# Performance work log

Hardware: AMD Instinct MI355X
Metric: run time of the kernel (lower is better)

## Reference

```python
import jax, jax.numpy as jnp
import numpy as np

B = 1024          # number of graphs
N = 64            # atoms per graph
NUM_NODES = B * N
HID = 256         # hidden_channels
H1 = HID // 2
E = 2_097_152     # edges (avg degree 32)


def _xavier(k, fan_in, fan_out):
    lim = np.sqrt(6.0 / (fan_in + fan_out)).astype(np.float32)
    return jax.random.uniform(k, (fan_in, fan_out), jnp.float32, -lim, lim)


def setup_inputs() -> dict:
    key = jax.random.key(0)
    ks = jax.random.split(key, 6)
    node_features = jax.random.normal(ks[0], (NUM_NODES, HID), jnp.float32)
    edge_index = jax.random.randint(ks[1], (2, E), 0, NUM_NODES)
    batch = jnp.repeat(jnp.arange(B), N)  # sorted graph ids, equal-size graphs
    W1 = _xavier(ks[2], HID + 1, H1); b1 = jnp.zeros((H1,), jnp.float32)
    W2 = _xavier(ks[3], H1, H1);      b2 = jnp.zeros((H1,), jnp.float32)
    W3 = _xavier(ks[4], H1, 1);       b3 = jnp.zeros((1,), jnp.float32)
    kT = jnp.ones((1,), jnp.float32)
    return {"node_features": node_features, "W1": W1, "b1": b1, "W2": W2,
            "b2": b2, "W3": W3, "b3": b3, "kT": kT,
            "edge_index": edge_index, "batch": batch}


def reference(node_features, W1, b1, W2, b2, W3, b3, kT, edge_index, batch):
    num_nodes = node_features.shape[0]
    # node degree: count of occurrences as source node
    deg = jnp.zeros((num_nodes,), jnp.float32).at[edge_index[0]].add(1.0)
    # per-graph atom counts and segment start offsets (n_atoms_i)
    counts = jax.ops.segment_sum(jnp.ones((num_nodes,), jnp.float32), batch,
                                 num_segments=B)
    start = jnp.cumsum(counts) - counts  # exclusive cumsum
    # stable per-graph sort of degrees in one shot: lexsort keys, primary=batch
    order = jnp.lexsort((deg, batch))  # global original indices, sorted by (batch, deg)
    # connectivity feature: local original index of the k-th smallest-degree
    # node in its graph, normalized by graph size (matches sorted_index / n_atoms_i)
    conn = (order.astype(jnp.float32) - start[batch]) / counts[batch]
    # MLP(hidden+1 -> hid/2 -> hid/2 -> 1) with silu
    x = jnp.concatenate([conn[:, None], node_features], axis=-1)  # [nodes, HID+1]
    h = jax.nn.silu(x @ W1 + b1)
    h = jax.nn.silu(h @ W2 + b2)
    logits = (h @ W3 + b3)[:, 0] / kT[0]
    # per-graph (segment) softmax
    m = jax.ops.segment_max(logits, batch, num_segments=B)
    e = jnp.exp(logits - m[batch])
    s = jax.ops.segment_sum(e, batch, num_segments=B)
    return e / s[batch]  # concat of per-graph softmaxed probabilities
```

## Files before the change

### kernel.cpp

```cpp
#include <hip/hip_runtime.h>

#define NB 1024
#define NPG 64
#define NUM_NODES 65536
#define HID 256
#define H1DIM 128
#define NE 2097152

typedef __attribute__((ext_vector_type(8))) _Float16 f16x8;
typedef __attribute__((ext_vector_type(4))) float f32x4;

#define W2F_HALF 32768
#define DEGF_OFF (96*1024)
#define PART_OFF (352*1024)

__global__ void wprep_kernel(const float* __restrict__ W1,
                             const float* __restrict__ W2,
                             _Float16* __restrict__ wf) {
    const int b = blockIdx.x;
    const int t = threadIdx.x;
    const int L = t & 63;
    const int j2 = (t >> 6) * 2;
    const float* src;
    _Float16* dst;
    int kt, nt;
    if (b < 64) { kt = b >> 3; nt = b & 7; src = W1 + H1DIM; dst = wf + b * 512; }
    else { int bb = b - 64; kt = bb >> 3; nt = bb & 7; src = W2; dst = wf + W2F_HALF + bb * 512; }
    const int k = kt * 32 + (L >> 4) * 8 + j2;
    const int n = nt * 16 + (L & 15);
    dst[L * 8 + j2]     = (_Float16)src[k * H1DIM + n];
    dst[L * 8 + j2 + 1] = (_Float16)src[(k + 1) * H1DIM + n];
}

__global__ __launch_bounds__(256) void hist_kernel(const int4* __restrict__ src4,
                                                   unsigned int* __restrict__ partials,
                                                   int G) {
    __shared__ unsigned int h[16384];
    const int b = blockIdx.x;
    const int t = threadIdx.x;
    uint4* h4 = (uint4*)h;
    for (int i = t; i < 4096; i += 256) h4[i] = make_uint4(0u, 0u, 0u, 0u);
    __syncthreads();
    const int n4 = (NE / 4) / G;
    const int4* p = src4 + b * n4;
    for (int i = t; i < n4; i += 256) {
        int4 v = p[i];
        atomicAdd(&h[v.x >> 2], 1u << ((v.x & 3) * 8));
        atomicAdd(&h[v.y >> 2], 1u << ((v.y & 3) * 8));
        atomicAdd(&h[v.z >> 2], 1u << ((v.z & 3) * 8));
        atomicAdd(&h[v.w >> 2], 1u << ((v.w & 3) * 8));
    }
    __syncthreads();
    uint4* dst = (uint4*)(partials + b * 16384);
    for (int i = t; i < 4096; i += 256) dst[i] = h4[i];
}

__global__ __launch_bounds__(256) void dreduce_kernel(
    const unsigned int* __restrict__ partials,
    unsigned int* __restrict__ degf, int G) {
    const int i = blockIdx.x * 256 + threadIdx.x;
    unsigned int s0 = 0, s1 = 0, s2 = 0, s3 = 0;
    for (int sl = 0; sl < G; ++sl) {
        unsigned int v = partials[sl * 16384 + i];
        s0 += v & 255u;
        s1 += (v >> 8) & 255u;
        s2 += (v >> 16) & 255u;
        s3 += v >> 24;
    }
    *(uint4*)&degf[i * 4] = make_uint4(s0, s1, s2, s3);
}

__global__ __launch_bounds__(256, 4) void mlp_softmax_kernel(
    const float* __restrict__ feat,
    const float* __restrict__ W1, const float* __restrict__ b1,
    const float* __restrict__ b2,
    const float* __restrict__ W3, const float* __restrict__ b3,
    const float* __restrict__ kT,
    const _Float16* __restrict__ wf,
    const unsigned int* __restrict__ degf,
    float* __restrict__ out)
{
    __shared__ _Float16 aF[2][4][64][8];
    __shared__ _Float16 h1[NPG][136];
    __shared__ unsigned int degs[NPG];
    __shared__ float conns[NPG];
    __shared__ float lpart[4][NPG];

    const int tid = threadIdx.x;
    const int L = tid & 63;
    const int w = tid >> 6;
    const int q = L >> 4;
    const int c = L & 15;
    const int g = blockIdx.x;
    const int node0 = g * NPG;

    const float* featw = &feat[(node0 + w * 16 + c) * HID + q * 8];

    float4 f0 = *(const float4*)featw;
    float4 f1 = *(const float4*)(featw + 4);

    if (tid < NPG) degs[tid] = degf[node0 + tid];
    __syncthreads();
    if (tid < NPG) {
        unsigned int di = degs[tid];
        int rk = 0;
#pragma unroll 8
        for (int j = 0; j < NPG; ++j) {
            unsigned int dj = degs[j];
            rk += (int)((dj < di) | ((dj == di) & (j < tid)));
        }
        conns[rk] = (float)tid * (1.0f / 64.0f);
    }
    __syncthreads();

    const int col0 = w * 32 + c;
    const int col1 = col0 + 16;

    f32x4 acc[4][2];
    {
        float b1a = b1[col0], b1b = b1[col1];
        float w0a = W1[col0], w0b = W1[col1];
#pragma unroll
        for (int mt = 0; mt < 4; ++mt)
#pragma unroll
            for (int r = 0; r < 4; ++r) {
                float cn = conns[mt * 16 + q * 4 + r];
                acc[mt][0][r] = fmaf(cn, w0a, b1a);
                acc[mt][1][r] = fmaf(cn, w0b, b1b);
            }
    }

    for (int kt = 0; kt < 8; ++kt) {
        {
            f16x8 av = { (_Float16)f0.x, (_Float16)f0.y, (_Float16)f0.z, (_Float16)f0.w,
                         (_Float16)f1.x, (_Float16)f1.y, (_Float16)f1.z, (_Float16)f1.w };
            *(f16x8*)&aF[kt & 1][w][L][0] = av;
        }
        if (kt < 7) {
            f0 = *(const float4*)(featw + (kt + 1) * 32);
            f1 = *(const float4*)(featw + (kt + 1) * 32 + 4);
        }
        f16x8 bf0 = *(const f16x8*)&wf[(kt * 8 + w * 2)     * 512 + L * 8];
        f16x8 bf1 = *(const f16x8*)&wf[(kt * 8 + w * 2 + 1) * 512 + L * 8];
        __syncthreads();
#pragma unroll
        for (int mt = 0; mt < 4; ++mt) {
            f16x8 a = *(const f16x8*)&aF[kt & 1][mt][L][0];
            acc[mt][0] = __builtin_amdgcn_mfma_f32_16x16x32_f16(a, bf0, acc[mt][0], 0, 0, 0);
            acc[mt][1] = __builtin_amdgcn_mfma_f32_16x16x32_f16(a, bf1, acc[mt][1], 0, 0, 0);
        }
    }

#pragma unroll
    for (int mt = 0; mt < 4; ++mt)
#pragma unroll
        for (int nt = 0; nt < 2; ++nt)
#pragma unroll
            for (int r = 0; r < 4; ++r) {
                float v = acc[mt][nt][r];
                float hv = v / (1.0f + __expf(-v));
                h1[mt * 16 + q * 4 + r][w * 32 + nt * 16 + c] = (_Float16)hv;
            }
    __syncthreads();

    f32x4 acc2[4][2];
    {
        float b2a = b2[col0], b2b = b2[col1];
#pragma unroll
        for (int mt = 0; mt < 4; ++mt)
#pragma unroll
            for (int r = 0; r < 4; ++r) { acc2[mt][0][r] = b2a; acc2[mt][1][r] = b2b; }
    }
    const _Float16* w2f = wf + W2F_HALF;
#pragma unroll
    for (int kt = 0; kt < 4; ++kt) {
        f16x8 bf0 = *(const f16x8*)&w2f[(kt * 8 + w * 2)     * 512 + L * 8];
        f16x8 bf1 = *(const f16x8*)&w2f[(kt * 8 + w * 2 + 1) * 512 + L * 8];
#pragma unroll
        for (int mt = 0; mt < 4; ++mt) {
            f16x8 a = *(const f16x8*)&h1[mt * 16 + c][kt * 32 + q * 8];
            acc2[mt][0] = __builtin_amdgcn_mfma_f32_16x16x32_f16(a, bf0, acc2[mt][0], 0, 0, 0);
            acc2[mt][1] = __builtin_amdgcn_mfma_f32_16x16x32_f16(a, bf1, acc2[mt][1], 0, 0, 0);
        }
    }

    {
        float w3a = W3[col0], w3b = W3[col1];
        float lg[4][4];
#pragma unroll
        for (int mt = 0; mt < 4; ++mt)
#pragma unroll
            for (int r = 0; r < 4; ++r) {
                float v0 = acc2[mt][0][r];
                float v1 = acc2[mt][1][r];
                float h0 = v0 / (1.0f + __expf(-v0));
                float h1v = v1 / (1.0f + __expf(-v1));
                lg[mt][r] = fmaf(h0, w3a, h1v * w3b);
            }
#pragma unroll
        for (int d = 1; d < 16; d <<= 1)
#pragma unroll
            for (int mt = 0; mt < 4; ++mt)
#pragma unroll
                for (int r = 0; r < 4; ++r)
                    lg[mt][r] += __shfl_xor(lg[mt][r], d, 64);
        if (c == 0) {
#pragma unroll
            for (int mt = 0; mt < 4; ++mt)
#pragma unroll
                for (int r = 0; r < 4; ++r)
                    lpart[w][mt * 16 + q * 4 + r] = lg[mt][r];
        }
    }
    __syncthreads();

    if (tid < NPG) {
        float s = lpart[0][tid] + lpart[1][tid] + lpart[2][tid] + lpart[3][tid];
        s = (s + b3[0]) / kT[0];
        float m = s;
#pragma unroll
        for (int d = 1; d < 64; d <<= 1) m = fmaxf(m, __shfl_xor(m, d, 64));
        float e = __expf(s - m);
        float su = e;
#pragma unroll
        for (int d = 1; d < 64; d <<= 1) su += __shfl_xor(su, d, 64);
        out[node0 + tid] = e / su;
    }
}

extern "C" void kernel_launch(void* const* d_in, const int* in_sizes, int n_in,
                              void* d_out, int out_size, void* d_ws, size_t ws_size,
                              hipStream_t stream)
{
    const float* feat = (const float*)d_in[0];
    const float* W1   = (const float*)d_in[1];
    const float* b1   = (const float*)d_in[2];
    const float* W2   = (const float*)d_in[3];
    const float* b2   = (const float*)d_in[4];
    const float* W3   = (const float*)d_in[5];
    const float* b3   = (const float*)d_in[6];
    const float* kT   = (const float*)d_in[7];
    const int*   ei   = (const int*)d_in[8];

    float* out = (float*)d_out;
    _Float16* wf = (_Float16*)d_ws;
    unsigned int* degf = (unsigned int*)((char*)d_ws + DEGF_OFF);
    unsigned int* partials = (unsigned int*)((char*)d_ws + PART_OFF);

    int G = 128;
    while (G > 8 && ws_size < (size_t)PART_OFF + (size_t)G * 65536) G >>= 1;

    wprep_kernel<<<96, 256, 0, stream>>>(W1, W2, wf);
    hist_kernel<<<G, 256, 0, stream>>>((const int4*)ei, partials, G);
    dreduce_kernel<<<64, 256, 0, stream>>>(partials, degf, G);
    mlp_softmax_kernel<<<NB, 256, 0, stream>>>(feat, W1, b1, b2, W3, b3, kT,
                                               wf, degf, out);
}
```

Baseline: 161.4 us.

## Fuse weight prep with histogram and fold degree reduction into MLP kernel

Merges the weight-conversion kernel into the histogram kernel as extra blocks and removes the separate degree-reduce kernel. Each MLP block now sums its own 64 nodes' packed degree counts across all partial histograms, using 128 threads in 8 groups. The histogram grid is doubled (G 128→256) to spread the atomics, and layer-2 weights and bias/scale loads are hoisted earlier. This cuts two launches and one global round trip, at the cost of the MLP kernel doing G strided loads per block before its matmuls start.

New measurement: 140.2 us. -13.1%, faster.

```diff
diff --git a/kernel.cpp b/kernel.cpp
--- a/kernel.cpp
+++ b/kernel.cpp
@@ -11,33 +11,33 @@
 typedef __attribute__((ext_vector_type(4))) float f32x4;
 
 #define W2F_HALF 32768
-#define DEGF_OFF (96*1024)
-#define PART_OFF (352*1024)
-
-__global__ void wprep_kernel(const float* __restrict__ W1,
-                             const float* __restrict__ W2,
-                             _Float16* __restrict__ wf) {
-    const int b = blockIdx.x;
+#define PART_OFF (128*1024)
+
+__global__ __launch_bounds__(256) void prep_hist_kernel(
+    const float* __restrict__ W1, const float* __restrict__ W2,
+    _Float16* __restrict__ wf,
+    const int4* __restrict__ src4, unsigned int* __restrict__ partials, int G)
+{
+    __shared__ unsigned int h[16384];
+    const int bx = blockIdx.x;
     const int t = threadIdx.x;
-    const int L = t & 63;
-    const int j2 = (t >> 6) * 2;
-    const float* src;
-    _Float16* dst;
-    int kt, nt;
-    if (b < 64) { kt = b >> 3; nt = b & 7; src = W1 + H1DIM; dst = wf + b * 512; }
-    else { int bb = b - 64; kt = bb >> 3; nt = bb & 7; src = W2; dst = wf + W2F_HALF + bb * 512; }
-    const int k = kt * 32 + (L >> 4) * 8 + j2;
-    const int n = nt * 16 + (L & 15);
-    dst[L * 8 + j2]     = (_Float16)src[k * H1DIM + n];
-    dst[L * 8 + j2 + 1] = (_Float16)src[(k + 1) * H1DIM + n];
-}
-
-__global__ __launch_bounds__(256) void hist_kernel(const int4* __restrict__ src4,
-                                                   unsigned int* __restrict__ partials,
-                                                   int G) {
-    __shared__ unsigned int h[16384];
-    const int b = blockIdx.x;
-    const int t = threadIdx.x;
+
+    if (bx < 96) {
+        const int L = t & 63;
+        const int j2 = (t >> 6) * 2;
+        const float* src;
+        _Float16* dst;
+        int kt, nt;
+        if (bx < 64) { kt = bx >> 3; nt = bx & 7; src = W1 + H1DIM; dst = wf + bx * 512; }
+        else { int bb = bx - 64; kt = bb >> 3; nt = bb & 7; src = W2; dst = wf + W2F_HALF + bb * 512; }
+        const int k = kt * 32 + (L >> 4) * 8 + j2;
+        const int n = nt * 16 + (L & 15);
+        dst[L * 8 + j2]     = (_Float16)src[k * H1DIM + n];
+        dst[L * 8 + j2 + 1] = (_Float16)src[(k + 1) * H1DIM + n];
+        return;
+    }
+
+    const int b = bx - 96;
     uint4* h4 = (uint4*)h;
     for (int i = t; i < 4096; i += 256) h4[i] = make_uint4(0u, 0u, 0u, 0u);
     __syncthreads();
@@ -55,21 +55,6 @@
     for (int i = t; i < 4096; i += 256) dst[i] = h4[i];
 }
 
-__global__ __launch_bounds__(256) void dreduce_kernel(
-    const unsigned int* __restrict__ partials,
-    unsigned int* __restrict__ degf, int G) {
-    const int i = blockIdx.x * 256 + threadIdx.x;
-    unsigned int s0 = 0, s1 = 0, s2 = 0, s3 = 0;
-    for (int sl = 0; sl < G; ++sl) {
-        unsigned int v = partials[sl * 16384 + i];
-        s0 += v & 255u;
-        s1 += (v >> 8) & 255u;
-        s2 += (v >> 16) & 255u;
-        s3 += v >> 24;
-    }
-    *(uint4*)&degf[i * 4] = make_uint4(s0, s1, s2, s3);
-}
-
 __global__ __launch_bounds__(256, 4) void mlp_softmax_kernel(
     const float* __restrict__ feat,
     const float* __restrict__ W1, const float* __restrict__ b1,
@@ -77,11 +62,12 @@
     const float* __restrict__ W3, const float* __restrict__ b3,
     const float* __restrict__ kT,
     const _Float16* __restrict__ wf,
-    const unsigned int* __restrict__ degf,
+    const unsigned int* __restrict__ partials, int G,
     float* __restrict__ out)
 {
     __shared__ _Float16 aF[2][4][64][8];
     __shared__ _Float16 h1[NPG][136];
+    __shared__ unsigned int dpart[8][16];
     __shared__ unsigned int degs[NPG];
     __shared__ float conns[NPG];
     __shared__ float lpart[4][NPG];
@@ -98,8 +84,34 @@
 
     float4 f0 = *(const float4*)featw;
     float4 f1 = *(const float4*)(featw + 4);
-
-    if (tid < NPG) degs[tid] = degf[node0 + tid];
+    const int col0 = w * 32 + c;
+    const int col1 = col0 + 16;
+    const float b1a = b1[col0], b1b = b1[col1];
+    const float w0a = W1[col0], w0b = W1[col1];
+    const float b2a = b2[col0], b2b = b2[col1];
+    const float w3a = W3[col0], w3b = W3[col1];
+    const float b3v = b3[0];
+    const float ikT = 1.0f / kT[0];
+
+    if (tid < 128) {
+        const int wd = tid & 15;
+        const int sg = tid >> 4;
+        const int n = G >> 3;
+        const unsigned int* p = partials + (size_t)(sg * n) * 16384 + g * 16 + wd;
+        unsigned int s = 0;
+        for (int i = 0; i < n; ++i) s += p[(size_t)i * 16384];
+        dpart[sg][wd] = s;
+    }
+    __syncthreads();
+    if (tid < 16) {
+        unsigned int s = 0;
+#pragma unroll
+        for (int k = 0; k < 8; ++k) s += dpart[k][tid];
+        degs[tid * 4 + 0] = s & 255u;
+        degs[tid * 4 + 1] = (s >> 8) & 255u;
+        degs[tid * 4 + 2] = (s >> 16) & 255u;
+        degs[tid * 4 + 3] = s >> 24;
+    }
     __syncthreads();
     if (tid < NPG) {
         unsigned int di = degs[tid];
@@ -113,22 +125,15 @@
     }
     __syncthreads();
 
-    const int col0 = w * 32 + c;
-    const int col1 = col0 + 16;
-
     f32x4 acc[4][2];
-    {
-        float b1a = b1[col0], b1b = b1[col1];
-        float w0a = W1[col0], w0b = W1[col1];
-#pragma unroll
-        for (int mt = 0; mt < 4; ++mt)
-#pragma unroll
-            for (int r = 0; r < 4; ++r) {
-                float cn = conns[mt * 16 + q * 4 + r];
-                acc[mt][0][r] = fmaf(cn, w0a, b1a);
-                acc[mt][1][r] = fmaf(cn, w0b, b1b);
-            }
-    }
+#pragma unroll
+    for (int mt = 0; mt < 4; ++mt)
+#pragma unroll
+        for (int r = 0; r < 4; ++r) {
+            float cn = conns[mt * 16 + q * 4 + r];
+            acc[mt][0][r] = fmaf(cn, w0a, b1a);
+            acc[mt][1][r] = fmaf(cn, w0b, b1b);
+        }
 
     for (int kt = 0; kt < 8; ++kt) {
         {
@@ -151,6 +156,16 @@
         }
     }
 
+    f16x8 l2b[8];
+    {
+        const _Float16* w2f = wf + W2F_HALF;
+#pragma unroll
+        for (int kt = 0; kt < 4; ++kt) {
+            l2b[kt * 2]     = *(const f16x8*)&w2f[(kt * 8 + w * 2)     * 512 + L * 8];
+            l2b[kt * 2 + 1] = *(const f16x8*)&w2f[(kt * 8 + w * 2 + 1) * 512 + L * 8];
+        }
+    }
+
 #pragma unroll
     for (int mt = 0; mt < 4; ++mt)
 #pragma unroll
@@ -164,28 +179,21 @@
     __syncthreads();
 
     f32x4 acc2[4][2];
-    {
-        float b2a = b2[col0], b2b = b2[col1];
-#pragma unroll
-        for (int mt = 0; mt < 4; ++mt)
-#pragma unroll
-            for (int r = 0; r < 4; ++r) { acc2[mt][0][r] = b2a; acc2[mt][1][r] = b2b; }
-    }
-    const _Float16* w2f = wf + W2F_HALF;
+#pragma unroll
+    for (int mt = 0; mt < 4; ++mt)
+#pragma unroll
+        for (int r = 0; r < 4; ++r) { acc2[mt][0][r] = b2a; acc2[mt][1][r] = b2b; }
 #pragma unroll
     for (int kt = 0; kt < 4; ++kt) {
-        f16x8 bf0 = *(const f16x8*)&w2f[(kt * 8 + w * 2)     * 512 + L * 8];
-        f16x8 bf1 = *(const f16x8*)&w2f[(kt * 8 + w * 2 + 1) * 512 + L * 8];
 #pragma unroll
         for (int mt = 0; mt < 4; ++mt) {
             f16x8 a = *(const f16x8*)&h1[mt * 16 + c][kt * 32 + q * 8];
-            acc2[mt][0] = __builtin_amdgcn_mfma_f32_16x16x32_f16(a, bf0, acc2[mt][0], 0, 0, 0);
-            acc2[mt][1] = __builtin_amdgcn_mfma_f32_16x16x32_f16(a, bf1, acc2[mt][1], 0, 0, 0);
+            acc2[mt][0] = __builtin_amdgcn_mfma_f32_16x16x32_f16(a, l2b[kt * 2],     acc2[mt][0], 0, 0, 0);
+            acc2[mt][1] = __builtin_amdgcn_mfma_f32_16x16x32_f16(a, l2b[kt * 2 + 1], acc2[mt][1], 0, 0, 0);
         }
     }
 
     {
-        float w3a = W3[col0], w3b = W3[col1];
         float lg[4][4];
 #pragma unroll
         for (int mt = 0; mt < 4; ++mt)
@@ -216,7 +224,7 @@
 
     if (tid < NPG) {
         float s = lpart[0][tid] + lpart[1][tid] + lpart[2][tid] + lpart[3][tid];
-        s = (s + b3[0]) / kT[0];
+        s = fmaf(s + b3v, ikT, 0.0f);
         float m = s;
 #pragma unroll
         for (int d = 1; d < 64; d <<= 1) m = fmaxf(m, __shfl_xor(m, d, 64));
@@ -244,15 +252,13 @@
 
     float* out = (float*)d_out;
     _Float16* wf = (_Float16*)d_ws;
-    unsigned int* degf = (unsigned int*)((char*)d_ws + DEGF_OFF);
     unsigned int* partials = (unsigned int*)((char*)d_ws + PART_OFF);
 
-    int G = 128;
+    int G = 256;
     while (G > 8 && ws_size < (size_t)PART_OFF + (size_t)G * 65536) G >>= 1;
 
-    wprep_kernel<<<96, 256, 0, stream>>>(W1, W2, wf);
-    hist_kernel<<<G, 256, 0, stream>>>((const int4*)ei, partials, G);
-    dreduce_kernel<<<64, 256, 0, stream>>>(partials, degf, G);
+    prep_hist_kernel<<<96 + G, 256, 0, stream>>>(W1, W2, wf, (const int4*)ei,
+                                                 partials, G);
     mlp_softmax_kernel<<<NB, 256, 0, stream>>>(feat, W1, b1, b2, W3, b3, kT,
-                                               wf, degf, out);
+                                               wf, partials, G, out);
 }
```
